# Performance work log

Measured on AMD Instinct MI355X. Metric: run time of the kernel, lower is better.

## Reference

```python
import jax, jax.numpy as jnp
import numpy as np

EPS = 1e-5

def layer_norm(x, alpha, beta):
    mean = jnp.mean(x, axis=-1, keepdims=True)
    var = jnp.mean(jnp.square(x - mean), axis=-1, keepdims=True)
    return alpha * ((x - mean) / jnp.sqrt(var + EPS)) + beta

def setup_inputs() -> dict:
    key = jax.random.key(0)
    B, S, D, H = 4, 2048, 1024, 16
    Dff = 4 * D
    ks = jax.random.split(key, 8)
    inp = {
        "x": jax.random.normal(ks[0], (B, S, D), jnp.float32),
        "attention_mask": jnp.ones((B, S), jnp.int32),
        "ln1_alpha": jnp.ones((D,), jnp.float32),
        "ln1_beta": jnp.zeros((D,), jnp.float32),
        "ln2_alpha": jnp.ones((D,), jnp.float32),
        "ln2_beta": jnp.zeros((D,), jnp.float32),
        "Wq": jax.random.normal(ks[1], (D, D), jnp.float32) * 0.05,
        "Wk": jax.random.normal(ks[2], (D, D), jnp.float32) * 0.05,
        "Wv": jax.random.normal(ks[3], (D, D), jnp.float32) * 0.05,
        "Wo": jax.random.normal(ks[4], (D, D), jnp.float32) * 0.05,
        "W1": jax.random.normal(ks[5], (D, Dff), jnp.float32) * 0.02,
        "b1": jnp.zeros((Dff,), jnp.float32),
        "W2": jax.random.normal(ks[6], (Dff, D), jnp.float32) * 0.02,
        "b2": jnp.zeros((D,), jnp.float32),
    }
    return inp

def reference(x, attention_mask, ln1_alpha, ln1_beta, ln2_alpha, ln2_beta,
              Wq, Wk, Wv, Wo, W1, b1, W2, b2):
    B, S, D = x.shape
    H = 16
    dh = D // H

    # LN1 + self-attention
    y = layer_norm(x, ln1_alpha, ln1_beta)
    Q = (y @ Wq).reshape(B, S, H, dh).transpose(0, 2, 1, 3)  # [B,H,S,dh]
    K = (y @ Wk).reshape(B, S, H, dh).transpose(0, 2, 1, 3)
    V = (y @ Wv).reshape(B, S, H, dh).transpose(0, 2, 1, 3)

    scores = jnp.einsum("bhqd,bhkd->bhqk", Q, K) / jnp.sqrt(jnp.float32(dh))
    causal = jnp.tril(jnp.ones((S, S), jnp.float32))  # [S,S]
    tmask = attention_mask.astype(jnp.float32)  # [B,S]
    amask = causal[None, None, :, :] * tmask[:, None, None, :] * tmask[:, None, :, None]
    scores = jnp.where(amask > 0, scores, jnp.float32(-1e30))
    attn = jax.nn.softmax(scores, axis=-1)
    # dropout omitted (deterministic inference)
    ctx = jnp.einsum("bhqk,bhkd->bhqd", attn, V)
    ctx = ctx.transpose(0, 2, 1, 3).reshape(B, S, D)
    x = x + ctx @ Wo

    # LN2 + GELU FFN
    y = layer_norm(x, ln2_alpha, ln2_beta)
    h = jax.nn.gelu(y @ W1 + b1, approximate=False)
    x = x + (h @ W2 + b2)
    return x
```

## Files before the change

kernel.cpp:

```cpp
#include <hip/hip_runtime.h>
#include <math.h>

typedef unsigned short u16;
typedef unsigned int u32;
typedef __attribute__((ext_vector_type(4))) unsigned short u16x4;
typedef __attribute__((ext_vector_type(8))) short bf16x8;
typedef __attribute__((ext_vector_type(4))) float f32x4;

#define B_ 4
#define S_ 2048
#define D_ 1024
#define H_ 16
#define NT (B_*S_)
#define DFF 4096

static __device__ __forceinline__ float bf2f(u16 u) {
    return __uint_as_float(((u32)u) << 16);
}
static __device__ __forceinline__ u16 f2bf(float f) {
    u32 u = __float_as_uint(f);
    u32 r = (u + 0x7fffu + ((u >> 16) & 1u)) >> 16;
    return (u16)r;
}
static __device__ __forceinline__ void gload_lds16(const void* g, void* l) {
    __builtin_amdgcn_global_load_lds(
        (const __attribute__((address_space(1))) void*)g,
        (__attribute__((address_space(3))) void*)l, 16, 0, 0);
}

__global__ void transpose_f2b4(const float* __restrict__ s0, const float* __restrict__ s1,
                               const float* __restrict__ s2, const float* __restrict__ s3,
                               u16* __restrict__ d0, u16* __restrict__ d1,
                               u16* __restrict__ d2, u16* __restrict__ d3,
                               int R, int C) {
    const float* in = s0; u16* out = d0;
    if (blockIdx.z == 1) { in = s1; out = d1; }
    else if (blockIdx.z == 2) { in = s2; out = d2; }
    else if (blockIdx.z == 3) { in = s3; out = d3; }
    __shared__ float t[32][33];
    int c0 = blockIdx.x * 32, r0 = blockIdx.y * 32;
    int x = threadIdx.x, y = threadIdx.y;
    #pragma unroll
    for (int i = 0; i < 4; i++)
        t[y + i*8][x] = in[(long)(r0 + y + i*8) * C + c0 + x];
    __syncthreads();
    #pragma unroll
    for (int i = 0; i < 4; i++)
        out[(long)(c0 + y + i*8) * R + r0 + x] = f2bf(t[x][y + i*8]);
}

__global__ void transpose_f2b(const float* __restrict__ in, u16* __restrict__ out,
                              int R, int C) {
    __shared__ float t[32][33];
    int c0 = blockIdx.x * 32, r0 = blockIdx.y * 32;
    int x = threadIdx.x, y = threadIdx.y;
    #pragma unroll
    for (int i = 0; i < 4; i++)
        t[y + i*8][x] = in[(long)(r0 + y + i*8) * C + c0 + x];
    __syncthreads();
    #pragma unroll
    for (int i = 0; i < 4; i++)
        out[(long)(c0 + y + i*8) * R + r0 + x] = f2bf(t[x][y + i*8]);
}

__global__ void transpose_v(const u16* __restrict__ V, u16* __restrict__ Vt) {
    __shared__ u16 t[32][33];
    int z = blockIdx.z; int b = z >> 4, h = z & 15;
    int s0 = blockIdx.x * 32, d0 = blockIdx.y * 32;
    int x = threadIdx.x, y = threadIdx.y;
    const u16* in = V + ((long)b * S_ + s0) * D_ + h * 64 + d0;
    #pragma unroll
    for (int i = 0; i < 4; i++)
        t[y + i*8][x] = in[(long)(y + i*8) * D_ + x];
    __syncthreads();
    u16* out = Vt + ((long)z * 64 + d0) * S_ + s0;
    #pragma unroll
    for (int i = 0; i < 4; i++)
        out[(long)(y + i*8) * S_ + x] = t[x][y + i*8];
}

__global__ __launch_bounds__(256) void ln_kernel(
    const float* __restrict__ X, const float* __restrict__ alpha,
    const float* __restrict__ beta, u16* __restrict__ Y) {
    int row = blockIdx.x, tid = threadIdx.x;
    float4 xv = ((const float4*)(X + (long)row * D_))[tid];
    float v[4] = {xv.x, xv.y, xv.z, xv.w};
    float s = 0.f, ss = 0.f;
    #pragma unroll
    for (int i = 0; i < 4; i++) { s += v[i]; ss += v[i]*v[i]; }
    #pragma unroll
    for (int off = 32; off >= 1; off >>= 1) {
        s += __shfl_xor(s, off);
        ss += __shfl_xor(ss, off);
    }
    __shared__ float red[8];
    __shared__ float stats[2];
    int w = tid >> 6;
    if ((tid & 63) == 0) { red[w] = s; red[4 + w] = ss; }
    __syncthreads();
    if (tid == 0) {
        float S = red[0] + red[1] + red[2] + red[3];
        float SS = red[4] + red[5] + red[6] + red[7];
        float mean = S * (1.f / D_);
        float var = SS * (1.f / D_) - mean * mean;
        stats[0] = mean; stats[1] = rsqrtf(var + 1e-5f);
    }
    __syncthreads();
    float mean = stats[0], rstd = stats[1];
    float4 av = ((const float4*)alpha)[tid];
    float4 bv = ((const float4*)beta)[tid];
    u16x4 o;
    o[0] = f2bf((v[0] - mean) * rstd * av.x + bv.x);
    o[1] = f2bf((v[1] - mean) * rstd * av.y + bv.y);
    o[2] = f2bf((v[2] - mean) * rstd * av.z + bv.z);
    o[3] = f2bf((v[3] - mean) * rstd * av.w + bv.w);
    *(u16x4*)(Y + (long)row * D_ + tid * 4) = o;
}

#define BM 128
#define BN 128
#define BK 64

__global__ __launch_bounds__(256, 2) void gemm_bt(
    const u16* __restrict__ A,
    const u16* __restrict__ Bt0, const u16* __restrict__ Bt1, const u16* __restrict__ Bt2,
    void* __restrict__ C0, void* __restrict__ C1, void* __restrict__ C2,
    int M, int N, int K, int mode,
    const float* __restrict__ bias, const float* __restrict__ resid) {
    const u16* Bt = Bt0; void* C = C0;
    if (blockIdx.z == 1) { Bt = Bt1; C = C1; }
    else if (blockIdx.z == 2) { Bt = Bt2; C = C2; }

    __shared__ __align__(16) u16 Asm[BM * BK];
    __shared__ __align__(16) u16 Bsm[BN * BK];

    int tid = threadIdx.x;
    int lane = tid & 63, wave = tid >> 6;
    int l15 = lane & 15, quad = lane >> 4;
    int wm = wave & 1, wn = wave >> 1;
    long tm0 = (long)blockIdx.y * BM, tn0 = (long)blockIdx.x * BN;

    int srow = lane >> 3;
    int scol = (lane & 7) * 8;

    f32x4 acc[4][4] = {};

    for (int k0 = 0; k0 < K; k0 += BK) {
        __syncthreads();
        #pragma unroll
        for (int c = 0; c < 4; c++) {
            int chunk = wave * 4 + c;
            int row = chunk * 8 + srow;
            gload_lds16(&A[(tm0 + row) * (long)K + k0 + scol], &Asm[chunk * 512]);
            gload_lds16(&Bt[(tn0 + row) * (long)K + k0 + scol], &Bsm[chunk * 512]);
        }
        __syncthreads();
        #pragma unroll
        for (int ks = 0; ks < 2; ks++) {
            bf16x8 af[4], bfm[4];
            #pragma unroll
            for (int mt = 0; mt < 4; mt++)
                af[mt] = *(const bf16x8*)&Asm[(wm*64 + mt*16 + l15) * BK + ks*32 + quad*8];
            #pragma unroll
            for (int nt = 0; nt < 4; nt++)
                bfm[nt] = *(const bf16x8*)&Bsm[(wn*64 + nt*16 + l15) * BK + ks*32 + quad*8];
            #pragma unroll
            for (int mt = 0; mt < 4; mt++)
                #pragma unroll
                for (int nt = 0; nt < 4; nt++)
                    acc[mt][nt] = __builtin_amdgcn_mfma_f32_16x16x32_bf16(
                        af[mt], bfm[nt], acc[mt][nt], 0, 0, 0);
        }
    }

    #pragma unroll
    for (int mt = 0; mt < 4; mt++) {
        #pragma unroll
        for (int nt = 0; nt < 4; nt++) {
            #pragma unroll
            for (int i = 0; i < 4; i++) {
                long r = tm0 + wm*64 + mt*16 + quad*4 + i;
                long cn = tn0 + wn*64 + nt*16 + l15;
                long idx = r * N + cn;
                float val = acc[mt][nt][i];
                if (mode == 0) {
                    ((u16*)C)[idx] = f2bf(val);
                } else if (mode == 1) {
                    ((float*)C)[idx] = val + resid[idx];
                } else if (mode == 2) {
                    val += bias[cn];
                    val = 0.5f * val * (1.0f + erff(val * 0.70710678118654752f));
                    ((u16*)C)[idx] = f2bf(val);
                } else {
                    ((float*)C)[idx] = val + bias[cn] + resid[idx];
                }
            }
        }
    }
}

#define LDP 72

__global__ __launch_bounds__(256, 2) void attn_kernel(
    const u16* __restrict__ Q, const u16* __restrict__ Kg, const u16* __restrict__ Vt,
    const int* __restrict__ mask, u16* __restrict__ O) {
    __shared__ __align__(16) u16 Psm[4][32 * LDP];
    int tid = threadIdx.x;
    int lane = tid & 63, wave = tid >> 6;
    int l15 = lane & 15, quad = lane >> 4;
    int bh = blockIdx.x; int b = bh >> 4, h = bh & 15;
    int j = wave * 8 + blockIdx.y;
    long tokBase = (long)b * S_;
    const float SCL = 0.125f * 1.4426950408889634f;
    const float MMAX = 20.0f;

    const bf16x8 ones = {16256,16256,16256,16256,16256,16256,16256,16256};
    u16* Pw = Psm[wave];
    const int* mb = mask + b * S_;

    #pragma unroll
    for (int half = 0; half < 2; half++) {
        int t = half ? (63 - j) : j;
        int q0 = t * 32;

        bf16x8 aq[2][2];
        #pragma unroll
        for (int mt = 0; mt < 2; mt++) {
            const u16* qptr = Q + (tokBase + q0 + mt*16 + l15) * D_ + h * 64;
            aq[mt][0] = *(const bf16x8*)(qptr + quad * 8);
            aq[mt][1] = *(const bf16x8*)(qptr + 32 + quad * 8);
        }

        f32x4 o[2][4] = {};
        f32x4 lacc[2] = {};
        int ktiles = t / 2 + 1;

        for (int kt = 0; kt < ktiles; kt++) {
            int k0 = kt * 64;
            bf16x8 kb[4][2], vb[4][2];
            #pragma unroll
            for (int nt = 0; nt < 4; nt++) {
                const u16* kp = Kg + (tokBase + k0 + nt*16 + l15) * D_ + h * 64;
                kb[nt][0] = *(const bf16x8*)(kp + quad * 8);
                kb[nt][1] = *(const bf16x8*)(kp + 32 + quad * 8);
            }
            #pragma unroll
            for (int d = 0; d < 4; d++) {
                const u16* vp = Vt + ((long)bh * 64 + d*16 + l15) * S_ + k0;
                vb[d][0] = *(const bf16x8*)(vp + quad * 8);
                vb[d][1] = *(const bf16x8*)(vp + 32 + quad * 8);
            }

            f32x4 s[2][4] = {};
            #pragma unroll
            for (int nt = 0; nt < 4; nt++) {
                s[0][nt] = __builtin_amdgcn_mfma_f32_16x16x32_bf16(aq[0][0], kb[nt][0], s[0][nt], 0,0,0);
                s[0][nt] = __builtin_amdgcn_mfma_f32_16x16x32_bf16(aq[0][1], kb[nt][1], s[0][nt], 0,0,0);
                s[1][nt] = __builtin_amdgcn_mfma_f32_16x16x32_bf16(aq[1][0], kb[nt][0], s[1][nt], 0,0,0);
                s[1][nt] = __builtin_amdgcn_mfma_f32_16x16x32_bf16(aq[1][1], kb[nt][1], s[1][nt], 0,0,0);
            }

            int mk = 0;
            #pragma unroll
            for (int nt = 0; nt < 4; nt++)
                if (mb[k0 + nt*16 + l15] != 0) mk |= (1 << nt);

            #pragma unroll
            for (int mt = 0; mt < 2; mt++) {
                #pragma unroll
                for (int i = 0; i < 4; i++) {
                    int qq = q0 + mt*16 + quad*4 + i;
                    #pragma unroll
                    for (int nt = 0; nt < 4; nt++) {
                        int kc = k0 + nt*16 + l15;
                        float p = exp2f(fmaf(s[mt][nt][i], SCL, -MMAX));
                        p = (kc <= qq && ((mk >> nt) & 1)) ? p : 0.f;
                        Pw[(mt*16 + quad*4 + i) * LDP + nt*16 + l15] = f2bf(p);
                    }
                }
            }
            asm volatile("s_waitcnt lgkmcnt(0)" ::: "memory");

            #pragma unroll
            for (int hv = 0; hv < 2; hv++) {
                bf16x8 ap0 = *(const bf16x8*)&Pw[l15 * LDP + hv*32 + quad*8];
                bf16x8 ap1 = *(const bf16x8*)&Pw[(16 + l15) * LDP + hv*32 + quad*8];
                #pragma unroll
                for (int d = 0; d < 4; d++) {
                    o[0][d] = __builtin_amdgcn_mfma_f32_16x16x32_bf16(ap0, vb[d][hv], o[0][d], 0,0,0);
                    o[1][d] = __builtin_amdgcn_mfma_f32_16x16x32_bf16(ap1, vb[d][hv], o[1][d], 0,0,0);
                }
                lacc[0] = __builtin_amdgcn_mfma_f32_16x16x32_bf16(ap0, ones, lacc[0], 0,0,0);
                lacc[1] = __builtin_amdgcn_mfma_f32_16x16x32_bf16(ap1, ones, lacc[1], 0,0,0);
            }
        }

        #pragma unroll
        for (int mt = 0; mt < 2; mt++) {
            #pragma unroll
            for (int i = 0; i < 4; i++) {
                float inv = 1.f / lacc[mt][i];
                long r = tokBase + q0 + mt*16 + quad*4 + i;
                #pragma unroll
                for (int d = 0; d < 4; d++)
                    O[r * D_ + h*64 + d*16 + l15] = f2bf(o[mt][d][i] * inv);
            }
        }
    }
}

extern "C" void kernel_launch(void* const* d_in, const int* in_sizes, int n_in,
                              void* d_out, int out_size, void* d_ws, size_t ws_size,
                              hipStream_t stream) {
    const float* x    = (const float*)d_in[0];
    const int*   am   = (const int*)d_in[1];
    const float* ln1a = (const float*)d_in[2];
    const float* ln1b = (const float*)d_in[3];
    const float* ln2a = (const float*)d_in[4];
    const float* ln2b = (const float*)d_in[5];
    const float* wq   = (const float*)d_in[6];
    const float* wk   = (const float*)d_in[7];
    const float* wv   = (const float*)d_in[8];
    const float* wo   = (const float*)d_in[9];
    const float* w1   = (const float*)d_in[10];
    const float* b1   = (const float*)d_in[11];
    const float* w2   = (const float*)d_in[12];
    const float* b2   = (const float*)d_in[13];
    float* out = (float*)d_out;

    char* ws = (char*)d_ws;
    const size_t MB16 = (size_t)16 * 1024 * 1024;
    u16* y1      = (u16*)(ws + 0 * MB16);
    u16* q       = (u16*)(ws + 1 * MB16);
    u16* k       = (u16*)(ws + 2 * MB16);
    u16* v       = (u16*)(ws + 3 * MB16);
    u16* wqt     = (u16*)(ws + 4 * MB16 + 0 * (size_t)D_ * D_ * 2);
    u16* wkt     = (u16*)(ws + 4 * MB16 + 1 * (size_t)D_ * D_ * 2);
    u16* wvt     = (u16*)(ws + 4 * MB16 + 2 * (size_t)D_ * D_ * 2);
    u16* wot     = (u16*)(ws + 4 * MB16 + 3 * (size_t)D_ * D_ * 2);
    u16* y2      = y1;
    u16* w1t     = q;
    u16* w2t     = q + (size_t)D_ * DFF;
    u16* h_full  = k;
    u16* ctx     = v;
    u16*   vt  = (u16*)d_out;
    float* x1f = out;

    dim3 tb(32, 8);
    transpose_f2b4<<<dim3(D_/32, D_/32, 4), tb, 0, stream>>>(
        wq, wk, wv, wo, wqt, wkt, wvt, wot, D_, D_);

    ln_kernel<<<NT, 256, 0, stream>>>(x, ln1a, ln1b, y1);

    gemm_bt<<<dim3(D_/BN, NT/BM, 3), 256, 0, stream>>>(
        y1, wqt, wkt, wvt, q, k, v, NT, D_, D_, 0, nullptr, nullptr);

    transpose_v<<<dim3(S_/32, 2, B_*H_), tb, 0, stream>>>(v, vt);

    attn_kernel<<<dim3(B_*H_, 8), 256, 0, stream>>>(q, k, vt, am, ctx);

    gemm_bt<<<dim3(D_/BN, NT/BM, 1), 256, 0, stream>>>(
        ctx, wot, wot, wot, x1f, x1f, x1f, NT, D_, D_, 1, nullptr, x);

    transpose_f2b<<<dim3(DFF/32, D_/32), tb, 0, stream>>>(w1, w1t, D_, DFF);
    transpose_f2b<<<dim3(D_/32, DFF/32), tb, 0, stream>>>(w2, w2t, DFF, D_);

    ln_kernel<<<NT, 256, 0, stream>>>(x1f, ln2a, ln2b, y2);

    gemm_bt<<<dim3(DFF/BN, NT/BM, 1), 256, 0, stream>>>(
        y2, w1t, w1t, w1t, h_full, h_full, h_full, NT, DFF, D_, 2, b1, nullptr);
    gemm_bt<<<dim3(D_/BN, NT/BM, 1), 256, 0, stream>>>(
        h_full, w2t, w2t, w2t, out, out, out, NT, D_, DFF, 3, b2, x1f);
}
```

Measured before the change: 691.0 us.

## Shrink attention query tile to 16 rows per wave and double grid

Each wave in the attention kernel now handles 16 query rows instead of 32, and the grid is doubled to 16 blocks per head with launch bounds raised to 4 blocks per CU. This gives more parallelism and finer causal load balancing. The QK^T product is computed transposed (K as the A operand), so each lane holds 4 consecutive keys for one query. That allows a vectorised int4 mask load and packed bf16 stores into LDS instead of scalar stores. The cost is that each K/V tile load is reused across half as many query rows, which raises global/L2 traffic per FLOP.

```diff
diff --git a/kernel.cpp b/kernel.cpp
--- a/kernel.cpp
+++ b/kernel.cpp
@@ -199,17 +199,17 @@
     }
 }
 
-#define LDP 72
-
-__global__ __launch_bounds__(256, 2) void attn_kernel(
+#define LDPq 72
+
+__global__ __launch_bounds__(256, 4) void attn_kernel(
     const u16* __restrict__ Q, const u16* __restrict__ Kg, const u16* __restrict__ Vt,
     const int* __restrict__ mask, u16* __restrict__ O) {
-    __shared__ __align__(16) u16 Psm[4][32 * LDP];
+    __shared__ __align__(16) u16 Psm[4][16 * LDPq];
     int tid = threadIdx.x;
     int lane = tid & 63, wave = tid >> 6;
     int l15 = lane & 15, quad = lane >> 4;
     int bh = blockIdx.x; int b = bh >> 4, h = bh & 15;
-    int j = wave * 8 + blockIdx.y;
+    int j = wave * 16 + blockIdx.y;
     long tokBase = (long)b * S_;
     const float SCL = 0.125f * 1.4426950408889634f;
     const float MMAX = 20.0f;
@@ -220,91 +220,75 @@
 
     #pragma unroll
     for (int half = 0; half < 2; half++) {
-        int t = half ? (63 - j) : j;
-        int q0 = t * 32;
-
-        bf16x8 aq[2][2];
-        #pragma unroll
-        for (int mt = 0; mt < 2; mt++) {
-            const u16* qptr = Q + (tokBase + q0 + mt*16 + l15) * D_ + h * 64;
-            aq[mt][0] = *(const bf16x8*)(qptr + quad * 8);
-            aq[mt][1] = *(const bf16x8*)(qptr + 32 + quad * 8);
-        }
-
-        f32x4 o[2][4] = {};
-        f32x4 lacc[2] = {};
-        int ktiles = t / 2 + 1;
+        int t = half ? (127 - j) : j;
+        int q0 = t * 16;
+
+        const u16* qptr = Q + (tokBase + q0 + l15) * D_ + h * 64;
+        bf16x8 aq0 = *(const bf16x8*)(qptr + quad * 8);
+        bf16x8 aq1 = *(const bf16x8*)(qptr + 32 + quad * 8);
+
+        f32x4 o[4] = {};
+        f32x4 lacc = {};
+        int qg = q0 + l15;
+        int ktiles = t / 4 + 1;
 
         for (int kt = 0; kt < ktiles; kt++) {
             int k0 = kt * 64;
             bf16x8 kb[4][2], vb[4][2];
             #pragma unroll
-            for (int nt = 0; nt < 4; nt++) {
-                const u16* kp = Kg + (tokBase + k0 + nt*16 + l15) * D_ + h * 64;
-                kb[nt][0] = *(const bf16x8*)(kp + quad * 8);
-                kb[nt][1] = *(const bf16x8*)(kp + 32 + quad * 8);
-            }
-            #pragma unroll
-            for (int d = 0; d < 4; d++) {
-                const u16* vp = Vt + ((long)bh * 64 + d*16 + l15) * S_ + k0;
-                vb[d][0] = *(const bf16x8*)(vp + quad * 8);
-                vb[d][1] = *(const bf16x8*)(vp + 32 + quad * 8);
-            }
-
-            f32x4 s[2][4] = {};
-            #pragma unroll
-            for (int nt = 0; nt < 4; nt++) {
-                s[0][nt] = __builtin_amdgcn_mfma_f32_16x16x32_bf16(aq[0][0], kb[nt][0], s[0][nt], 0,0,0);
-                s[0][nt] = __builtin_amdgcn_mfma_f32_16x16x32_bf16(aq[0][1], kb[nt][1], s[0][nt], 0,0,0);
-                s[1][nt] = __builtin_amdgcn_mfma_f32_16x16x32_bf16(aq[1][0], kb[nt][0], s[1][nt], 0,0,0);
-                s[1][nt] = __builtin_amdgcn_mfma_f32_16x16x32_bf16(aq[1][1], kb[nt][1], s[1][nt], 0,0,0);
-            }
-
-            int mk = 0;
-            #pragma unroll
-            for (int nt = 0; nt < 4; nt++)
-                if (mb[k0 + nt*16 + l15] != 0) mk |= (1 << nt);
-
-            #pragma unroll
-            for (int mt = 0; mt < 2; mt++) {
-                #pragma unroll
-                for (int i = 0; i < 4; i++) {
-                    int qq = q0 + mt*16 + quad*4 + i;
-                    #pragma unroll
-                    for (int nt = 0; nt < 4; nt++) {
-                        int kc = k0 + nt*16 + l15;
-                        float p = exp2f(fmaf(s[mt][nt][i], SCL, -MMAX));
-                        p = (kc <= qq && ((mk >> nt) & 1)) ? p : 0.f;
-                        Pw[(mt*16 + quad*4 + i) * LDP + nt*16 + l15] = f2bf(p);
-                    }
-                }
+            for (int st = 0; st < 4; st++) {
+                const u16* kp = Kg + (tokBase + k0 + st*16 + l15) * D_ + h * 64;
+                kb[st][0] = *(const bf16x8*)(kp + quad * 8);
+                kb[st][1] = *(const bf16x8*)(kp + 32 + quad * 8);
+            }
+            #pragma unroll
+            for (int dt = 0; dt < 4; dt++) {
+                const u16* vp = Vt + ((long)bh * 64 + dt*16 + l15) * S_ + k0;
+                vb[dt][0] = *(const bf16x8*)(vp + quad * 8);
+                vb[dt][1] = *(const bf16x8*)(vp + 32 + quad * 8);
+            }
+
+            f32x4 s[4] = {};
+            #pragma unroll
+            for (int st = 0; st < 4; st++) {
+                s[st] = __builtin_amdgcn_mfma_f32_16x16x32_bf16(kb[st][0], aq0, s[st], 0,0,0);
+                s[st] = __builtin_amdgcn_mfma_f32_16x16x32_bf16(kb[st][1], aq1, s[st], 0,0,0);
+            }
+
+            #pragma unroll
+            for (int st = 0; st < 4; st++) {
+                int4 m4 = *(const int4*)&mb[k0 + st*16 + quad*4];
+                int kbase = k0 + st*16 + quad*4;
+                float p[4];
+                p[0] = (kbase + 0 <= qg && m4.x != 0) ? exp2f(fmaf(s[st][0], SCL, -MMAX)) : 0.f;
+                p[1] = (kbase + 1 <= qg && m4.y != 0) ? exp2f(fmaf(s[st][1], SCL, -MMAX)) : 0.f;
+                p[2] = (kbase + 2 <= qg && m4.z != 0) ? exp2f(fmaf(s[st][2], SCL, -MMAX)) : 0.f;
+                p[3] = (kbase + 3 <= qg && m4.w != 0) ? exp2f(fmaf(s[st][3], SCL, -MMAX)) : 0.f;
+                u32 pk0 = __builtin_amdgcn_perm(__float_as_uint(p[1]), __float_as_uint(p[0]), 0x07060302u);
+                u32 pk1 = __builtin_amdgcn_perm(__float_as_uint(p[3]), __float_as_uint(p[2]), 0x07060302u);
+                uint2 w2 = {pk0, pk1};
+                *(uint2*)&Pw[l15 * LDPq + st*16 + quad*4] = w2;
             }
             asm volatile("s_waitcnt lgkmcnt(0)" ::: "memory");
-
-            #pragma unroll
-            for (int hv = 0; hv < 2; hv++) {
-                bf16x8 ap0 = *(const bf16x8*)&Pw[l15 * LDP + hv*32 + quad*8];
-                bf16x8 ap1 = *(const bf16x8*)&Pw[(16 + l15) * LDP + hv*32 + quad*8];
-                #pragma unroll
-                for (int d = 0; d < 4; d++) {
-                    o[0][d] = __builtin_amdgcn_mfma_f32_16x16x32_bf16(ap0, vb[d][hv], o[0][d], 0,0,0);
-                    o[1][d] = __builtin_amdgcn_mfma_f32_16x16x32_bf16(ap1, vb[d][hv], o[1][d], 0,0,0);
-                }
-                lacc[0] = __builtin_amdgcn_mfma_f32_16x16x32_bf16(ap0, ones, lacc[0], 0,0,0);
-                lacc[1] = __builtin_amdgcn_mfma_f32_16x16x32_bf16(ap1, ones, lacc[1], 0,0,0);
-            }
+            bf16x8 ap0 = *(const bf16x8*)&Pw[l15 * LDPq + quad*8];
+            bf16x8 ap1 = *(const bf16x8*)&Pw[l15 * LDPq + 32 + quad*8];
+
+            #pragma unroll
+            for (int dt = 0; dt < 4; dt++) {
+                o[dt] = __builtin_amdgcn_mfma_f32_16x16x32_bf16(ap0, vb[dt][0], o[dt], 0,0,0);
+                o[dt] = __builtin_amdgcn_mfma_f32_16x16x32_bf16(ap1, vb[dt][1], o[dt], 0,0,0);
+            }
+            lacc = __builtin_amdgcn_mfma_f32_16x16x32_bf16(ap0, ones, lacc, 0,0,0);
+            lacc = __builtin_amdgcn_mfma_f32_16x16x32_bf16(ap1, ones, lacc, 0,0,0);
         }
 
         #pragma unroll
-        for (int mt = 0; mt < 2; mt++) {
-            #pragma unroll
-            for (int i = 0; i < 4; i++) {
-                float inv = 1.f / lacc[mt][i];
-                long r = tokBase + q0 + mt*16 + quad*4 + i;
-                #pragma unroll
-                for (int d = 0; d < 4; d++)
-                    O[r * D_ + h*64 + d*16 + l15] = f2bf(o[mt][d][i] * inv);
-            }
+        for (int i = 0; i < 4; i++) {
+            float inv = 1.f / lacc[i];
+            long r = tokBase + q0 + quad*4 + i;
+            #pragma unroll
+            for (int dt = 0; dt < 4; dt++)
+                O[r * D_ + h*64 + dt*16 + l15] = f2bf(o[dt][i] * inv);
         }
     }
 }
@@ -357,7 +341,7 @@
 
     transpose_v<<<dim3(S_/32, 2, B_*H_), tb, 0, stream>>>(v, vt);
 
-    attn_kernel<<<dim3(B_*H_, 8), 256, 0, stream>>>(q, k, vt, am, ctx);
+    attn_kernel<<<dim3(B_*H_, 16), 256, 0, stream>>>(q, k, vt, am, ctx);
 
     gemm_bt<<<dim3(D_/BN, NT/BM, 1), 256, 0, stream>>>(
         ctx, wot, wot, wot, x1f, x1f, x1f, NT, D_, D_, 1, nullptr, x);
```

Result: slower. 774.1 us (+12.0%).

## Double-buffer K/V loads and split causal tiles in attention kernel

Applied to the files above, without the earlier changes.

The attention inner loop now software-pipelines K, V and mask loads into two register buffer sets, so the next tile's global loads overlap the current tile's MFMA work. Fully unmasked tiles skip per-element causal checks, and only the diagonal tile applies them. The key-padding mask is precomputed into an additive float bias by a small new kernel and folded into the exp2 argument. The S tile is computed transposed so probabilities pack with perm into bf16 pairs and are written to shared memory as vector stores. The cost is more registers from the doubled buffers, which could lower occupancy, plus one extra small launch.

```diff
diff --git a/kernel.cpp b/kernel.cpp
--- a/kernel.cpp
+++ b/kernel.cpp
@@ -77,6 +77,11 @@
     #pragma unroll
     for (int i = 0; i < 4; i++)
         out[(long)(y + i*8) * S_ + x] = t[x][y + i*8];
+}
+
+__global__ void mask_bias_k(const int* __restrict__ am, float* __restrict__ mb) {
+    int i = blockIdx.x * 256 + threadIdx.x;
+    mb[i] = am[i] ? -20.0f : -10020.0f;
 }
 
 __global__ __launch_bounds__(256) void ln_kernel(
@@ -203,7 +208,7 @@
 
 __global__ __launch_bounds__(256, 2) void attn_kernel(
     const u16* __restrict__ Q, const u16* __restrict__ Kg, const u16* __restrict__ Vt,
-    const int* __restrict__ mask, u16* __restrict__ O) {
+    const float* __restrict__ maskb, u16* __restrict__ O) {
     __shared__ __align__(16) u16 Psm[4][32 * LDP];
     int tid = threadIdx.x;
     int lane = tid & 63, wave = tid >> 6;
@@ -212,98 +217,162 @@
     int j = wave * 8 + blockIdx.y;
     long tokBase = (long)b * S_;
     const float SCL = 0.125f * 1.4426950408889634f;
-    const float MMAX = 20.0f;
 
     const bf16x8 ones = {16256,16256,16256,16256,16256,16256,16256,16256};
     u16* Pw = Psm[wave];
-    const int* mb = mask + b * S_;
+    const float* mbias_b = maskb + b * S_;
+    const u16* Kbase = Kg + (tokBase + l15) * D_ + h * 64;
+    const u16* Vbase = Vt + ((long)bh * 64 + l15) * S_;
 
     #pragma unroll
     for (int half = 0; half < 2; half++) {
         int t = half ? (63 - j) : j;
         int q0 = t * 32;
+        int nf = t >> 1;
+        int r0 = nf * 64;
+        bool todd = (t & 1) != 0;
+        int qg0 = q0 + l15, qg1 = q0 + 16 + l15;
 
         bf16x8 aq[2][2];
         #pragma unroll
-        for (int mt = 0; mt < 2; mt++) {
-            const u16* qptr = Q + (tokBase + q0 + mt*16 + l15) * D_ + h * 64;
-            aq[mt][0] = *(const bf16x8*)(qptr + quad * 8);
-            aq[mt][1] = *(const bf16x8*)(qptr + 32 + quad * 8);
+        for (int qh = 0; qh < 2; qh++) {
+            const u16* qptr = Q + (tokBase + q0 + qh*16 + l15) * D_ + h * 64;
+            aq[qh][0] = *(const bf16x8*)(qptr + quad * 8);
+            aq[qh][1] = *(const bf16x8*)(qptr + 32 + quad * 8);
         }
 
         f32x4 o[2][4] = {};
         f32x4 lacc[2] = {};
-        int ktiles = t / 2 + 1;
-
-        for (int kt = 0; kt < ktiles; kt++) {
-            int k0 = kt * 64;
-            bf16x8 kb[4][2], vb[4][2];
-            #pragma unroll
-            for (int nt = 0; nt < 4; nt++) {
-                const u16* kp = Kg + (tokBase + k0 + nt*16 + l15) * D_ + h * 64;
-                kb[nt][0] = *(const bf16x8*)(kp + quad * 8);
-                kb[nt][1] = *(const bf16x8*)(kp + 32 + quad * 8);
-            }
-            #pragma unroll
-            for (int d = 0; d < 4; d++) {
-                const u16* vp = Vt + ((long)bh * 64 + d*16 + l15) * S_ + k0;
-                vb[d][0] = *(const bf16x8*)(vp + quad * 8);
-                vb[d][1] = *(const bf16x8*)(vp + 32 + quad * 8);
-            }
-
+
+        bf16x8 ka[4][2], va[4][2], kb2[4][2], vb2[4][2];
+        float4 ma[4], mb2[4];
+
+        auto load_kv = [&](bf16x8 (&KB)[4][2], bf16x8 (&VB)[4][2],
+                           float4 (&MB)[4], int K0) {
+            #pragma unroll
+            for (int st = 0; st < 4; st++) {
+                const u16* kp = Kbase + (long)(K0 + st*16) * D_;
+                KB[st][0] = *(const bf16x8*)(kp + quad * 8);
+                KB[st][1] = *(const bf16x8*)(kp + 32 + quad * 8);
+                MB[st] = *(const float4*)&mbias_b[K0 + st*16 + quad*4];
+            }
+            #pragma unroll
+            for (int dt = 0; dt < 4; dt++) {
+                const u16* vp = Vbase + (long)(dt*16) * S_ + K0;
+                VB[dt][0] = *(const bf16x8*)(vp + quad * 8);
+                VB[dt][1] = *(const bf16x8*)(vp + 32 + quad * 8);
+            }
+        };
+
+        auto pv_accum = [&](bf16x8 (&VB)[4][2]) {
+            asm volatile("s_waitcnt lgkmcnt(0)" ::: "memory");
+            #pragma unroll
+            for (int qh = 0; qh < 2; qh++) {
+                bf16x8 ap0 = *(const bf16x8*)&Pw[(qh*16 + l15) * LDP + quad*8];
+                bf16x8 ap1 = *(const bf16x8*)&Pw[(qh*16 + l15) * LDP + 32 + quad*8];
+                #pragma unroll
+                for (int dt = 0; dt < 4; dt++) {
+                    o[qh][dt] = __builtin_amdgcn_mfma_f32_16x16x32_bf16(ap0, VB[dt][0], o[qh][dt], 0,0,0);
+                    o[qh][dt] = __builtin_amdgcn_mfma_f32_16x16x32_bf16(ap1, VB[dt][1], o[qh][dt], 0,0,0);
+                }
+                lacc[qh] = __builtin_amdgcn_mfma_f32_16x16x32_bf16(ap0, ones, lacc[qh], 0,0,0);
+                lacc[qh] = __builtin_amdgcn_mfma_f32_16x16x32_bf16(ap1, ones, lacc[qh], 0,0,0);
+            }
+        };
+
+        auto compute_full = [&](bf16x8 (&KB)[4][2], bf16x8 (&VB)[4][2],
+                                float4 (&MB)[4]) {
             f32x4 s[2][4] = {};
             #pragma unroll
-            for (int nt = 0; nt < 4; nt++) {
-                s[0][nt] = __builtin_amdgcn_mfma_f32_16x16x32_bf16(aq[0][0], kb[nt][0], s[0][nt], 0,0,0);
-                s[0][nt] = __builtin_amdgcn_mfma_f32_16x16x32_bf16(aq[0][1], kb[nt][1], s[0][nt], 0,0,0);
-                s[1][nt] = __builtin_amdgcn_mfma_f32_16x16x32_bf16(aq[1][0], kb[nt][0], s[1][nt], 0,0,0);
-                s[1][nt] = __builtin_amdgcn_mfma_f32_16x16x32_bf16(aq[1][1], kb[nt][1], s[1][nt], 0,0,0);
-            }
-
-            int mk = 0;
-            #pragma unroll
-            for (int nt = 0; nt < 4; nt++)
-                if (mb[k0 + nt*16 + l15] != 0) mk |= (1 << nt);
-
-            #pragma unroll
-            for (int mt = 0; mt < 2; mt++) {
-                #pragma unroll
-                for (int i = 0; i < 4; i++) {
-                    int qq = q0 + mt*16 + quad*4 + i;
+            for (int st = 0; st < 4; st++) {
+                #pragma unroll
+                for (int qh = 0; qh < 2; qh++) {
+                    s[qh][st] = __builtin_amdgcn_mfma_f32_16x16x32_bf16(KB[st][0], aq[qh][0], s[qh][st], 0,0,0);
+                    s[qh][st] = __builtin_amdgcn_mfma_f32_16x16x32_bf16(KB[st][1], aq[qh][1], s[qh][st], 0,0,0);
+                }
+            }
+            #pragma unroll
+            for (int st = 0; st < 4; st++) {
+                #pragma unroll
+                for (int qh = 0; qh < 2; qh++) {
+                    float p0 = __builtin_amdgcn_exp2f(fmaf(s[qh][st][0], SCL, MB[st].x));
+                    float p1 = __builtin_amdgcn_exp2f(fmaf(s[qh][st][1], SCL, MB[st].y));
+                    float p2 = __builtin_amdgcn_exp2f(fmaf(s[qh][st][2], SCL, MB[st].z));
+                    float p3 = __builtin_amdgcn_exp2f(fmaf(s[qh][st][3], SCL, MB[st].w));
+                    u32 pk0 = __builtin_amdgcn_perm(__float_as_uint(p1), __float_as_uint(p0), 0x07060302u);
+                    u32 pk1 = __builtin_amdgcn_perm(__float_as_uint(p3), __float_as_uint(p2), 0x07060302u);
+                    uint2 wv = {pk0, pk1};
+                    *(uint2*)&Pw[(qh*16 + l15) * LDP + st*16 + quad*4] = wv;
+                }
+            }
+            pv_accum(VB);
+        };
+
+        auto compute_rem = [&](bf16x8 (&KB)[4][2], bf16x8 (&VB)[4][2],
+                               float4 (&MB)[4]) {
+            f32x4 s[2][4] = {};
+            int nst = todd ? 4 : 2;
+            for (int st = 0; st < nst; st++) {
+                #pragma unroll
+                for (int qh = 0; qh < 2; qh++) {
+                    s[qh][st] = __builtin_amdgcn_mfma_f32_16x16x32_bf16(KB[st][0], aq[qh][0], s[qh][st], 0,0,0);
+                    s[qh][st] = __builtin_amdgcn_mfma_f32_16x16x32_bf16(KB[st][1], aq[qh][1], s[qh][st], 0,0,0);
+                }
+            }
+            for (int st = 0; st < nst; st++) {
+                bool causal = todd ? (st >= 2) : true;
+                int kbq = r0 + st*16 + quad*4;
+                #pragma unroll
+                for (int qh = 0; qh < 2; qh++) {
+                    int qg = qh ? qg1 : qg0;
+                    float p0 = __builtin_amdgcn_exp2f(fmaf(s[qh][st][0], SCL, MB[st].x));
+                    float p1 = __builtin_amdgcn_exp2f(fmaf(s[qh][st][1], SCL, MB[st].y));
+                    float p2 = __builtin_amdgcn_exp2f(fmaf(s[qh][st][2], SCL, MB[st].z));
+                    float p3 = __builtin_amdgcn_exp2f(fmaf(s[qh][st][3], SCL, MB[st].w));
+                    if (causal) {
+                        p0 = (kbq + 0 <= qg) ? p0 : 0.f;
+                        p1 = (kbq + 1 <= qg) ? p1 : 0.f;
+                        p2 = (kbq + 2 <= qg) ? p2 : 0.f;
+                        p3 = (kbq + 3 <= qg) ? p3 : 0.f;
+                    }
+                    u32 pk0 = __builtin_amdgcn_perm(__float_as_uint(p1), __float_as_uint(p0), 0x07060302u);
+                    u32 pk1 = __builtin_amdgcn_perm(__float_as_uint(p3), __float_as_uint(p2), 0x07060302u);
+                    uint2 wv = {pk0, pk1};
+                    *(uint2*)&Pw[(qh*16 + l15) * LDP + st*16 + quad*4] = wv;
+                }
+            }
+            if (!todd) {
+                uint2 z2 = {0u, 0u};
+                #pragma unroll
+                for (int st = 2; st < 4; st++)
                     #pragma unroll
-                    for (int nt = 0; nt < 4; nt++) {
-                        int kc = k0 + nt*16 + l15;
-                        float p = exp2f(fmaf(s[mt][nt][i], SCL, -MMAX));
-                        p = (kc <= qq && ((mk >> nt) & 1)) ? p : 0.f;
-                        Pw[(mt*16 + quad*4 + i) * LDP + nt*16 + l15] = f2bf(p);
-                    }
-                }
-            }
-            asm volatile("s_waitcnt lgkmcnt(0)" ::: "memory");
-
-            #pragma unroll
-            for (int hv = 0; hv < 2; hv++) {
-                bf16x8 ap0 = *(const bf16x8*)&Pw[l15 * LDP + hv*32 + quad*8];
-                bf16x8 ap1 = *(const bf16x8*)&Pw[(16 + l15) * LDP + hv*32 + quad*8];
-                #pragma unroll
-                for (int d = 0; d < 4; d++) {
-                    o[0][d] = __builtin_amdgcn_mfma_f32_16x16x32_bf16(ap0, vb[d][hv], o[0][d], 0,0,0);
-                    o[1][d] = __builtin_amdgcn_mfma_f32_16x16x32_bf16(ap1, vb[d][hv], o[1][d], 0,0,0);
-                }
-                lacc[0] = __builtin_amdgcn_mfma_f32_16x16x32_bf16(ap0, ones, lacc[0], 0,0,0);
-                lacc[1] = __builtin_amdgcn_mfma_f32_16x16x32_bf16(ap1, ones, lacc[1], 0,0,0);
-            }
-        }
+                    for (int qh = 0; qh < 2; qh++)
+                        *(uint2*)&Pw[(qh*16 + l15) * LDP + st*16 + quad*4] = z2;
+            }
+            pv_accum(VB);
+        };
+
+        load_kv(ka, va, ma, 0);
+        for (int kt = 0; kt < nf; kt += 2) {
+            load_kv(kb2, vb2, mb2, (kt + 1) * 64);
+            compute_full(ka, va, ma);
+            if (kt + 1 < nf) {
+                load_kv(ka, va, ma, (kt + 2) * 64);
+                compute_full(kb2, vb2, mb2);
+            }
+        }
+        if (nf & 1) compute_rem(kb2, vb2, mb2);
+        else        compute_rem(ka, va, ma);
 
         #pragma unroll
-        for (int mt = 0; mt < 2; mt++) {
+        for (int qh = 0; qh < 2; qh++) {
             #pragma unroll
             for (int i = 0; i < 4; i++) {
-                float inv = 1.f / lacc[mt][i];
-                long r = tokBase + q0 + mt*16 + quad*4 + i;
-                #pragma unroll
-                for (int d = 0; d < 4; d++)
-                    O[r * D_ + h*64 + d*16 + l15] = f2bf(o[mt][d][i] * inv);
+                float inv = 1.f / lacc[qh][i];
+                long r = tokBase + q0 + qh*16 + quad*4 + i;
+                #pragma unroll
+                for (int dt = 0; dt < 4; dt++)
+                    O[r * D_ + h*64 + dt*16 + l15] = f2bf(o[qh][dt][i] * inv);
             }
         }
     }
@@ -344,6 +413,7 @@
     u16* h_full  = k;
     u16* ctx     = v;
     u16*   vt  = (u16*)d_out;
+    float* mbias = (float*)((char*)d_out + 24 * 1024 * 1024);
     float* x1f = out;
 
     dim3 tb(32, 8);
@@ -356,8 +426,9 @@
         y1, wqt, wkt, wvt, q, k, v, NT, D_, D_, 0, nullptr, nullptr);
 
     transpose_v<<<dim3(S_/32, 2, B_*H_), tb, 0, stream>>>(v, vt);
-
-    attn_kernel<<<dim3(B_*H_, 8), 256, 0, stream>>>(q, k, vt, am, ctx);
+    mask_bias_k<<<dim3(NT/256), 256, 0, stream>>>(am, mbias);
+
+    attn_kernel<<<dim3(B_*H_, 8), 256, 0, stream>>>(q, k, vt, mbias, ctx);
 
     gemm_bt<<<dim3(D_/BN, NT/BM, 1), 256, 0, stream>>>(
         ctx, wot, wot, wot, x1f, x1f, x1f, NT, D_, D_, 1, nullptr, x);
```

Result: slower. 815.2 us (+18.0%).
